# Optimization experiments

Measured on AMD Instinct MI355X. Metric: run time of the kernel, lower is better.

Reference implementation:

```python
import jax, jax.numpy as jnp
import numpy as np

N = 50000      # batch_num_nodes
E = 800000     # num edges (~avg degree 16)
A = 16         # num_atom_types
H = 64         # hidden dim
Z = 32         # latent dim
L_ENC = 2
L_DEC = 2
C_NORM = 16.0  # coordinate-update normalization (avg degree)


def _glorot(key, shape):
    fan = shape[-2] + shape[-1]
    return jax.random.normal(key, shape, dtype=jnp.float32) * np.float32(np.sqrt(2.0 / fan))


def _make_stack(key, n_layers, h_dim):
    # Stacked per-layer EGNN params: edge MLP (2 layers), coord head, node MLP (2 layers).
    def one(k):
        k0, k1, k2, k3, k4 = jax.random.split(k, 5)
        return (_glorot(k0, (2 * h_dim + 1, h_dim)), jnp.zeros((h_dim,), jnp.float32),
                _glorot(k1, (h_dim, h_dim)), jnp.zeros((h_dim,), jnp.float32),
                _glorot(k2, (h_dim, 1)),
                _glorot(k3, (2 * h_dim, h_dim)), jnp.zeros((h_dim,), jnp.float32),
                _glorot(k4, (h_dim, h_dim)), jnp.zeros((h_dim,), jnp.float32))
    parts = [one(k) for k in jax.random.split(key, n_layers)]
    return tuple(jnp.stack(p) for p in zip(*parts))


PARAM_NAMES = ["We1", "be1", "We2", "be2", "Wx", "Wn1", "bn1", "Wn2", "bn2"]


def setup_inputs() -> dict:
    key = jax.random.key(0)
    k = jax.random.split(key, 10)
    h = jax.random.normal(k[0], (N, A), dtype=jnp.float32)
    x = jax.random.normal(k[1], (N, 3), dtype=jnp.float32)
    edge_index = jax.random.randint(k[2], (2, E), 0, N, dtype=jnp.int32)
    inp = {"h": h, "x": x, "edge_index": edge_index,
           "W_emb": _glorot(k[3], (A, H)), "b_emb": jnp.zeros((H,), jnp.float32),
           "W_lat": _glorot(k[4], (H, Z)), "b_lat": jnp.zeros((Z,), jnp.float32),
           "W_up": _glorot(k[5], (Z, H)), "b_up": jnp.zeros((H,), jnp.float32),
           "W_out": _glorot(k[6], (H, A)), "b_out": jnp.zeros((A,), jnp.float32)}
    for n, p in zip(PARAM_NAMES, _make_stack(k[7], L_ENC, H)):
        inp["enc_" + n] = p
    for n, p in zip(PARAM_NAMES, _make_stack(k[8], L_DEC, H)):
        inp["dec_" + n] = p
    return inp


def _egnn_layer(h, x, src, dst, We1, be1, We2, be2, Wx, Wn1, bn1, Wn2, bn2):
    rel = x[src] - x[dst]                                    # [E, 3] gather
    d2 = jnp.sum(rel * rel, axis=-1, keepdims=True)          # [E, 1]
    ef = jnp.concatenate([h[src], h[dst], d2], axis=-1)      # [E, 2H+1]
    m = jax.nn.silu(jax.nn.silu(ef @ We1 + be1) @ We2 + be2)  # [E, H] per-edge message
    # equivariant coordinate update: scatter-add weighted relative vectors
    x = x + jax.ops.segment_sum(rel * (m @ Wx), dst, num_segments=N) / C_NORM
    agg = jnp.asarray(jax.ops.segment_sum(m, dst, num_segments=N))  # [N, H]
    h = h + jax.nn.silu(jnp.concatenate([h, agg], axis=-1) @ Wn1 + bn1) @ Wn2 + bn2
    return h, x


def reference(h, x, edge_index, W_emb, b_emb, W_lat, b_lat, W_up, b_up, W_out, b_out,
              enc_We1, enc_be1, enc_We2, enc_be2, enc_Wx, enc_Wn1, enc_bn1, enc_Wn2, enc_bn2,
              dec_We1, dec_be1, dec_We2, dec_be2, dec_Wx, dec_Wn1, dec_bn1, dec_Wn2, dec_bn2):
    src, dst = edge_index[0], edge_index[1]
    hh = h @ W_emb + b_emb
    for i in range(L_ENC):
        hh, x = _egnn_layer(hh, x, src, dst,
                            enc_We1[i], enc_be1[i], enc_We2[i], enc_be2[i], enc_Wx[i],
                            enc_Wn1[i], enc_bn1[i], enc_Wn2[i], enc_bn2[i])
    z = hh @ W_lat + b_lat                                   # latent [N, Z]
    hh = z @ W_up + b_up
    for i in range(L_DEC):
        hh, x = _egnn_layer(hh, x, src, dst,
                            dec_We1[i], dec_be1[i], dec_We2[i], dec_be2[i], dec_Wx[i],
                            dec_Wn1[i], dec_bn1[i], dec_Wn2[i], dec_bn2[i])
    h_rec = hh @ W_out + b_out                               # reconstructed atom-type logits
    return jnp.concatenate([h_rec, x], axis=-1)              # [N, A+3]
```

## Files before the change

### kernel.cpp

```cpp
#include <hip/hip_runtime.h>

#define NN 50000
#define NE 800000
#define MAXC 100000
#define EBLK 1024
#define SCB ((NN + 255) / 256)

__device__ __forceinline__ float silu_f(float v) {
    return v * __builtin_amdgcn_rcpf(1.f + __expf(-v));
}

typedef __bf16 bf16;
typedef bf16 v8bf __attribute__((ext_vector_type(8)));
typedef float v4f __attribute__((ext_vector_type(4)));

#define UNPACK8(dstv, ptr) { \
    float4 _a = reinterpret_cast<const float4*>(ptr)[0]; \
    float4 _b = reinterpret_cast<const float4*>(ptr)[1]; \
    dstv[0]=_a.x; dstv[1]=_a.y; dstv[2]=_a.z; dstv[3]=_a.w; \
    dstv[4]=_b.x; dstv[5]=_b.y; dstv[6]=_b.z; dstv[7]=_b.w; }

__global__ __launch_bounds__(256) void k_embed(
    const float* __restrict__ h_in, const float* __restrict__ x_in,
    const float* __restrict__ W, const float* __restrict__ b,
    float* __restrict__ h, float* __restrict__ xp)
{
    int t = blockIdx.x * 256 + threadIdx.x;
    if (t < NN * 4) { int n = t >> 2, c = t & 3; xp[t] = (c < 3) ? x_in[n * 3 + c] : 0.f; }
    int n = t >> 6, j = t & 63;
    const float* hr = h_in + n * 16;
    float acc = b[j];
#pragma unroll
    for (int k = 0; k < 16; k++) acc = fmaf(hr[k], W[k * 64 + j], acc);
    h[t] = acc;
}

__global__ __launch_bounds__(256) void k_prep_all(
    const float* __restrict__ eW1, const float* __restrict__ dW1,
    const float* __restrict__ eW2, const float* __restrict__ dW2,
    const float* __restrict__ eN1, const float* __restrict__ dN1,
    const float* __restrict__ eN2, const float* __restrict__ dN2,
    const float* __restrict__ Wlat, const float* __restrict__ Wup,
    bf16* __restrict__ We1h, bf16* __restrict__ We1l,
    bf16* __restrict__ We2h, bf16* __restrict__ We2l,
    bf16* __restrict__ Wn1h, bf16* __restrict__ Wn1l,
    bf16* __restrict__ Wn2h, bf16* __restrict__ Wn2l,
    bf16* __restrict__ Wlh,  bf16* __restrict__ Wll,
    bf16* __restrict__ Wuh,  bf16* __restrict__ Wul)
{
    int t = blockIdx.x * 256 + threadIdx.x;
    float w; int di; bf16 *Wh, *Wl;
    if (t < 98304) {
        const float *encW, *decW; int K, stride; int r;
        if (t < 32768)      { r = t;         encW = eW1; decW = dW1; K = 128; stride = 129 * 64; Wh = We1h; Wl = We1l; }
        else if (t < 49152) { r = t - 32768; encW = eW2; decW = dW2; K = 64;  stride = 64 * 64;  Wh = We2h; Wl = We2l; }
        else if (t < 81920) { r = t - 49152; encW = eN1; decW = dN1; K = 128; stride = 128 * 64; Wh = Wn1h; Wl = Wn1l; }
        else                { r = t - 81920; encW = eN2; decW = dN2; K = 64;  stride = 64 * 64;  Wh = Wn2h; Wl = Wn2l; }
        int per = K * 64;
        int li = r / per, rr = r - li * per;
        int k = rr >> 6, col = rr & 63;
        const float* Wsrc = (li < 2 ? encW : decW) + (li & 1) * stride;
        w = Wsrc[k * 64 + col];
        int kh = k >> 5, gg = (k >> 3) & 3, b = k & 7;
        di = li * per + (((kh * 4 + gg) * 64 + col) * 8 + b);
    } else if (t < 100352) {
        int r = t - 98304;
        int k = r >> 5, col = r & 31;
        w = Wlat[k * 32 + col];
        int kh = k >> 5, gg = (k >> 3) & 3, b = k & 7;
        di = ((kh * 4 + gg) * 32 + col) * 8 + b;
        Wh = Wlh; Wl = Wll;
    } else {
        int r = t - 100352;
        int k = r >> 6, col = r & 63;
        w = Wup[k * 64 + col];
        int gg = (k >> 3) & 3, b = k & 7;
        di = (gg * 64 + col) * 8 + b;
        Wh = Wuh; Wl = Wul;
    }
    bf16 hi = (bf16)w;
    Wh[di] = hi; Wl[di] = (bf16)(w - (float)hi);
}

__global__ __launch_bounds__(256) void k_zero_cnt(int* __restrict__ cnt)
{
    int t = blockIdx.x * 256 + threadIdx.x;
    if (t <= NN) cnt[t] = 0;
}

__global__ __launch_bounds__(256) void k_hist(const int* __restrict__ dst, int* __restrict__ cnt)
{
    int e = blockIdx.x * 256 + threadIdx.x;
    if (e < NE) atomicAdd(&cnt[dst[e]], 1);
}

__global__ __launch_bounds__(256) void k_blocksum(
    const int* __restrict__ cnt, int* __restrict__ bsum)
{
    int b = blockIdx.x, tid = threadIdx.x;
    int i = b * 256 + tid;
    int deg = (i < NN) ? cnt[i] : 0;
    int chk = (deg + 15) >> 4;
#pragma unroll
    for (int d = 1; d < 64; d <<= 1) { deg += __shfl_xor(deg, d); chk += __shfl_xor(chk, d); }
    __shared__ int sd[4], sc[4];
    int wv = tid >> 6;
    if ((tid & 63) == 0) { sd[wv] = deg; sc[wv] = chk; }
    __syncthreads();
    if (tid == 0) {
        bsum[b] = sd[0] + sd[1] + sd[2] + sd[3];
        bsum[SCB + b] = sc[0] + sc[1] + sc[2] + sc[3];
    }
}

__global__ __launch_bounds__(256) void k_scanbase(
    const int* __restrict__ bsum, int* __restrict__ bbase, int* __restrict__ ncptr)
{
    __shared__ int s[256], s2[256];
    int tid = threadIdx.x;
    int v  = (tid < SCB) ? bsum[tid] : 0;
    int v2 = (tid < SCB) ? bsum[SCB + tid] : 0;
    s[tid] = v; s2[tid] = v2;
    __syncthreads();
    for (int d = 1; d < 256; d <<= 1) {
        int u  = (tid >= d) ? s[tid - d] : 0;
        int u2 = (tid >= d) ? s2[tid - d] : 0;
        __syncthreads();
        s[tid] += u; s2[tid] += u2;
        __syncthreads();
    }
    if (tid < SCB) {
        bbase[tid]       = s[tid] - v;
        bbase[SCB + tid] = s2[tid] - v2;
    }
    if (tid == 255) *ncptr = s2[SCB - 1];
}

__global__ __launch_bounds__(256) void k_applyscan(
    int* __restrict__ cnt, const int* __restrict__ bbase,
    int* __restrict__ off, int* __restrict__ cur, int2* __restrict__ cpair)
{
    int b = blockIdx.x, tid = threadIdx.x;
    int i = b * 256 + tid;
    int deg = (i < NN) ? cnt[i] : 0;
    int chk = (deg + 15) >> 4;
    __shared__ int s[256], s2[256];
    s[tid] = deg; s2[tid] = chk;
    __syncthreads();
    for (int d = 1; d < 256; d <<= 1) {
        int u  = (tid >= d) ? s[tid - d] : 0;
        int u2 = (tid >= d) ? s2[tid - d] : 0;
        __syncthreads();
        s[tid] += u; s2[tid] += u2;
        __syncthreads();
    }
    if (i < NN) {
        int o = bbase[b] + s[tid] - deg;
        off[i] = o; cur[i] = o;
        int co = bbase[SCB + b] + s2[tid] - chk;
        int e = o + deg;
        int single = (deg <= 16) ? (1 << 25) : 0;
        for (int eb = o; eb < e; eb += 16) {
            int c = min(e - eb, 16);
            cpair[co++] = make_int2(i, eb | (c << 20) | single);
        }
    }
    if (i == 0) off[NN] = NE;
}

__global__ __launch_bounds__(256) void k_scatter(
    const int* __restrict__ dst, const int* __restrict__ srcArr,
    int* __restrict__ cur, int* __restrict__ srcp)
{
    int e = blockIdx.x * 256 + threadIdx.x;
    if (e < NE) { int p = atomicAdd(&cur[dst[e]], 1); srcp[p] = srcArr[e]; }
}

__global__ __launch_bounds__(256) void k_pq_mfma(
    const float* __restrict__ h,
    const bf16* __restrict__ We1h, const bf16* __restrict__ We1l,
    const float* __restrict__ be1,
    float* __restrict__ P, float* __restrict__ Q,
    float* __restrict__ agg, float* __restrict__ dxb)
{
    const int wv = threadIdx.x >> 6, lane = threadIdx.x & 63;
    const int g = lane >> 4, l15 = lane & 15;
    const int n0 = (blockIdx.x * 4 + wv) * 16;
    if (n0 >= NN) return;
    const int nrow = n0 + l15;

    v8bf Ah[2], Al[2];
#pragma unroll
    for (int kh = 0; kh < 2; kh++) {
        float v[8];
        UNPACK8(v, h + nrow * 64 + kh * 32 + g * 8);
#pragma unroll
        for (int b = 0; b < 8; b++) {
            bf16 hi = (bf16)v[b];
            Ah[kh][b] = hi; Al[kh][b] = (bf16)(v[b] - (float)hi);
        }
    }

    const v8bf* Bh = reinterpret_cast<const v8bf*>(We1h);
    const v8bf* Bl = reinterpret_cast<const v8bf*>(We1l);

    float be1v[4];
#pragma unroll
    for (int nt = 0; nt < 4; nt++) be1v[nt] = be1[l15 + 16 * nt];

#pragma unroll
    for (int nt = 0; nt < 4; nt++) {
        v4f ap = {0.f,0.f,0.f,0.f}, aq = {0.f,0.f,0.f,0.f};
#pragma unroll
        for (int kh = 0; kh < 2; kh++) {
            int fiP = (kh * 4 + g) * 64 + l15 + 16 * nt;
            int fiQ = ((kh + 2) * 4 + g) * 64 + l15 + 16 * nt;
            v8bf bph = Bh[fiP], bpl = Bl[fiP];
            v8bf bqh = Bh[fiQ], bql = Bl[fiQ];
            ap = __builtin_amdgcn_mfma_f32_16x16x32_bf16(Ah[kh], bph, ap, 0, 0, 0);
            ap = __builtin_amdgcn_mfma_f32_16x16x32_bf16(Ah[kh], bpl, ap, 0, 0, 0);
            ap = __builtin_amdgcn_mfma_f32_16x16x32_bf16(Al[kh], bph, ap, 0, 0, 0);
            aq = __builtin_amdgcn_mfma_f32_16x16x32_bf16(Ah[kh], bqh, aq, 0, 0, 0);
            aq = __builtin_amdgcn_mfma_f32_16x16x32_bf16(Ah[kh], bql, aq, 0, 0, 0);
            aq = __builtin_amdgcn_mfma_f32_16x16x32_bf16(Al[kh], bqh, aq, 0, 0, 0);
        }
#pragma unroll
        for (int i = 0; i < 4; i++) {
            int ro = (n0 + g * 4 + i) * 64 + l15 + 16 * nt;
            P[ro] = ap[i] + be1v[nt];
            Q[ro] = aq[i];
            agg[ro] = 0.f;
        }
    }
    {
        int nd = lane >> 2, cc = lane & 3;
        if (cc < 3) dxb[(n0 + nd) * 3 + cc] = 0.f;
    }
}

__device__ __forceinline__ void edge_compute(
    int n, int ct, int sg,
    const float4& xn, const float4& xs,
    const float4* pw, const float4* qv4,
    const v8bf* __restrict__ BHf, const v8bf* __restrict__ BLf,
    const float (&wdv)[2][8], const float (&be2v)[4], const float (&wxv)[4],
    int g, int l15, int lane,
    float* __restrict__ agg, float* __restrict__ dxb)
{
    float rx = xs.x - xn.x, ry = xs.y - xn.y, rz = xs.z - xn.z;
    float d2 = rx * rx + ry * ry + rz * rz;
    const float* pv = reinterpret_cast<const float*>(pw);
    const float* qv = reinterpret_cast<const float*>(qv4);

    v8bf Ah[2], Al[2];
#pragma unroll
    for (int kh = 0; kh < 2; kh++) {
#pragma unroll
        for (int b = 0; b < 8; b++) {
            float m1 = silu_f(pv[kh * 8 + b] + qv[kh * 8 + b] + d2 * wdv[kh][b]);
            bf16 hi = (bf16)m1;
            Ah[kh][b] = hi;
            Al[kh][b] = (bf16)(m1 - (float)hi);
        }
    }

    v4f acc[4];
#pragma unroll
    for (int nt = 0; nt < 4; nt++) {
        v4f a = {0.f, 0.f, 0.f, 0.f};
#pragma unroll
        for (int kh = 0; kh < 2; kh++) {
            int fi = (kh * 4 + g) * 64 + l15 + 16 * nt;
            v8bf bh = BHf[fi], bl = BLf[fi];
            a = __builtin_amdgcn_mfma_f32_16x16x32_bf16(Ah[kh], bh, a, 0, 0, 0);
            a = __builtin_amdgcn_mfma_f32_16x16x32_bf16(Ah[kh], bl, a, 0, 0, 0);
            a = __builtin_amdgcn_mfma_f32_16x16x32_bf16(Al[kh], bh, a, 0, 0, 0);
        }
        acc[nt] = a;
    }

    float aggv[4] = {0.f, 0.f, 0.f, 0.f};
    float dxx = 0.f, dxy = 0.f, dxz = 0.f;
#pragma unroll
    for (int i = 0; i < 4; i++) {
        bool valid = (g * 4 + i) < ct;
        float m0 = silu_f(acc[0][i] + be2v[0]); m0 = valid ? m0 : 0.f;
        float m1 = silu_f(acc[1][i] + be2v[1]); m1 = valid ? m1 : 0.f;
        float m2 = silu_f(acc[2][i] + be2v[2]); m2 = valid ? m2 : 0.f;
        float m3 = silu_f(acc[3][i] + be2v[3]); m3 = valid ? m3 : 0.f;
        aggv[0] += m0; aggv[1] += m1; aggv[2] += m2; aggv[3] += m3;
        float pd = m0 * wxv[0] + m1 * wxv[1] + m2 * wxv[2] + m3 * wxv[3];
        pd += __shfl_xor(pd, 1); pd += __shfl_xor(pd, 2);
        pd += __shfl_xor(pd, 4); pd += __shfl_xor(pd, 8);
        float rxe = __shfl(rx, g * 4 + i);
        float rye = __shfl(ry, g * 4 + i);
        float rze = __shfl(rz, g * 4 + i);
        if (l15 == 0) { dxx += rxe * pd; dxy += rye * pd; dxz += rze * pd; }
    }

#pragma unroll
    for (int nt = 0; nt < 4; nt++) {
        aggv[nt] += __shfl_xor(aggv[nt], 16);
        aggv[nt] += __shfl_xor(aggv[nt], 32);
    }
    if (lane < 16) {
        if (sg) {
#pragma unroll
            for (int nt = 0; nt < 4; nt++) agg[n * 64 + l15 + 16 * nt] = aggv[nt];
        } else {
#pragma unroll
            for (int nt = 0; nt < 4; nt++) unsafeAtomicAdd(&agg[n * 64 + l15 + 16 * nt], aggv[nt]);
        }
    }
    dxx += __shfl_xor(dxx, 16); dxx += __shfl_xor(dxx, 32);
    dxy += __shfl_xor(dxy, 16); dxy += __shfl_xor(dxy, 32);
    dxz += __shfl_xor(dxz, 16); dxz += __shfl_xor(dxz, 32);
    if (lane == 0) {
        if (sg) {
            dxb[n * 3 + 0] = dxx; dxb[n * 3 + 1] = dxy; dxb[n * 3 + 2] = dxz;
        } else {
            unsafeAtomicAdd(&dxb[n * 3 + 0], dxx);
            unsafeAtomicAdd(&dxb[n * 3 + 1], dxy);
            unsafeAtomicAdd(&dxb[n * 3 + 2], dxz);
        }
    }
}

__global__ __launch_bounds__(256) void k_edge_pipe(
    const int* __restrict__ srcp, const int2* __restrict__ cpair, const int* __restrict__ ncptr,
    const float* __restrict__ xp,
    const float* __restrict__ P, const float* __restrict__ Q,
    const float* __restrict__ Wd,
    const bf16* __restrict__ We2h, const bf16* __restrict__ We2l,
    const float* __restrict__ be2, const float* __restrict__ Wx,
    float* __restrict__ agg, float* __restrict__ dxb)
{
    const int wv = threadIdx.x >> 6, lane = threadIdx.x & 63;
    const int g = lane >> 4, l15 = lane & 15;
    const int Wstride = EBLK * 4;
    const int NC = *ncptr;
    int c0 = blockIdx.x * 4 + wv;
    if (c0 >= NC) return;

    const float4* xp4 = reinterpret_cast<const float4*>(xp);
    const float4* Pf4 = reinterpret_cast<const float4*>(P);
    const float4* Qf4 = reinterpret_cast<const float4*>(Q);
    const v8bf* BHf = reinterpret_cast<const v8bf*>(We2h);
    const v8bf* BLf = reinterpret_cast<const v8bf*>(We2l);

    float wdv[2][8];
    UNPACK8(wdv[0], Wd + g * 8);
    UNPACK8(wdv[1], Wd + 32 + g * 8);
    float be2v[4], wxv[4];
#pragma unroll
    for (int nt = 0; nt < 4; nt++) { be2v[nt] = be2[l15 + 16 * nt]; wxv[nt] = Wx[l15 + 16 * nt]; }

    int c1 = c0 + Wstride, c2 = c1 + Wstride, c3 = c2 + Wstride;
    int2 m0 = cpair[c0];
    int2 m1 = cpair[min(c1, NC - 1)];
    int2 m2 = cpair[min(c2, NC - 1)];
    int n0 = m0.x, eb0 = m0.y & 0xFFFFF, ct0 = (m0.y >> 20) & 31, sg0 = (m0.y >> 25) & 1;
    int n1 = m1.x, eb1 = m1.y & 0xFFFFF, ct1 = (m1.y >> 20) & 31, sg1 = (m1.y >> 25) & 1;
    int s0 = srcp[eb0 + min(l15, ct0 - 1)];
    int s1 = srcp[eb1 + min(l15, ct1 - 1)];
    float4 xn0 = xp4[n0], xn1 = xp4[n1];
    float4 xs0 = xp4[s0];
    float4 pw0[4], qv0[4];
    pw0[0] = Pf4[s0 * 16 + g * 2];     pw0[1] = Pf4[s0 * 16 + g * 2 + 1];
    pw0[2] = Pf4[s0 * 16 + 8 + g * 2]; pw0[3] = Pf4[s0 * 16 + 8 + g * 2 + 1];
    qv0[0] = Qf4[n0 * 16 + g * 2];     qv0[1] = Qf4[n0 * 16 + g * 2 + 1];
    qv0[2] = Qf4[n0 * 16 + 8 + g * 2]; qv0[3] = Qf4[n0 * 16 + 8 + g * 2 + 1];

    while (true) {
        float4 xs1 = xp4[s1];
        float4 pw1[4], qv1[4];
        pw1[0] = Pf4[s1 * 16 + g * 2];     pw1[1] = Pf4[s1 * 16 + g * 2 + 1];
        pw1[2] = Pf4[s1 * 16 + 8 + g * 2]; pw1[3] = Pf4[s1 * 16 + 8 + g * 2 + 1];
        qv1[0] = Qf4[n1 * 16 + g * 2];     qv1[1] = Qf4[n1 * 16 + g * 2 + 1];
        qv1[2] = Qf4[n1 * 16 + 8 + g * 2]; qv1[3] = Qf4[n1 * 16 + 8 + g * 2 + 1];
        int n2 = m2.x, eb2 = m2.y & 0xFFFFF, ct2 = (m2.y >> 20) & 31, sg2 = (m2.y >> 25) & 1;
        int s2 = srcp[eb2 + min(l15, ct2 - 1)];
        float4 xn2 = xp4[n2];
        int2 m3 = cpair[min(c3, NC - 1)];

        edge_compute(n0, ct0, sg0, xn0, xs0, pw0, qv0,
                     BHf, BLf, wdv, be2v, wxv, g, l15, lane, agg, dxb);

        c0 = c1; c1 = c2; c2 = c3; c3 += Wstride;
        n0 = n1; ct0 = ct1; sg0 = sg1; xn0 = xn1; xs0 = xs1;
#pragma unroll
        for (int j = 0; j < 4; j++) { pw0[j] = pw1[j]; qv0[j] = qv1[j]; }
        n1 = n2; ct1 = ct2; sg1 = sg2; s1 = s2; xn1 = xn2;
        m2 = m3;
        if (c0 >= NC) break;
    }
}

__global__ __launch_bounds__(256) void k_node_mfma(
    float* __restrict__ h, float* __restrict__ xp,
    float* __restrict__ agg, const float* __restrict__ dxb,
    const bf16* __restrict__ Wn1h, const bf16* __restrict__ Wn1l, const float* __restrict__ bn1,
    const bf16* __restrict__ Wn2h, const bf16* __restrict__ Wn2l, const float* __restrict__ bn2,
    int do_pq,
    const bf16* __restrict__ We1nh, const bf16* __restrict__ We1nl, const float* __restrict__ be1n,
    float* __restrict__ P, float* __restrict__ Q, float* __restrict__ dxbz,
    int do_lat,
    const bf16* __restrict__ Wlh, const bf16* __restrict__ Wll, const float* __restrict__ bl,
    const bf16* __restrict__ Wuh, const bf16* __restrict__ Wul, const float* __restrict__ bu)
{
    __shared__ float sh[4][16][68];
    __shared__ float su[4][16][68];

    const int wv = threadIdx.x >> 6, lane = threadIdx.x & 63;
    const int g = lane >> 4, l15 = lane & 15;
    const int n0 = (blockIdx.x * 4 + wv) * 16;
    if (n0 >= NN) return;

    const int nrow = n0 + l15;

    v8bf Ah[4], Al[4];
#pragma unroll
    for (int kh = 0; kh < 2; kh++) {
        float v[8];
        UNPACK8(v, h + nrow * 64 + kh * 32 + g * 8);
        *reinterpret_cast<float4*>(&sh[wv][l15][kh * 32 + g * 8])     = *reinterpret_cast<const float4*>(&v[0]);
        *reinterpret_cast<float4*>(&sh[wv][l15][kh * 32 + g * 8 + 4]) = *reinterpret_cast<const float4*>(&v[4]);
#pragma unroll
        for (int b = 0; b < 8; b++) {
            bf16 hi = (bf16)v[b];
            Ah[kh][b] = hi; Al[kh][b] = (bf16)(v[b] - (float)hi);
        }
    }
#pragma unroll
    for (int kh = 0; kh < 2; kh++) {
        float v[8];
        UNPACK8(v, agg + nrow * 64 + kh * 32 + g * 8);
#pragma unroll
        for (int b = 0; b < 8; b++) {
            bf16 hi = (bf16)v[b];
            Ah[2 + kh][b] = hi; Al[2 + kh][b] = (bf16)(v[b] - (float)hi);
        }
    }

    const v8bf* B1h = reinterpret_cast<const v8bf*>(Wn1h);
    const v8bf* B1l = reinterpret_cast<const v8bf*>(Wn1l);
    const v8bf* B2h = reinterpret_cast<const v8bf*>(Wn2h);
    const v8bf* B2l = reinterpret_cast<const v8bf*>(Wn2l);

    float bn1v[4];
#pragma unroll
    for (int nt = 0; nt < 4; nt++) bn1v[nt] = bn1[l15 + 16 * nt];
#pragma unroll
    for (int nt = 0; nt < 4; nt++) {
        v4f a = {0.f, 0.f, 0.f, 0.f};
#pragma unroll
        for (int kh = 0; kh < 4; kh++) {
            int fi = (kh * 4 + g) * 64 + l15 + 16 * nt;
            v8bf bh = B1h[fi], bl_ = B1l[fi];
            a = __builtin_amdgcn_mfma_f32_16x16x32_bf16(Ah[kh], bh, a, 0, 0, 0);
            a = __builtin_amdgcn_mfma_f32_16x16x32_bf16(Ah[kh], bl_, a, 0, 0, 0);
            a = __builtin_amdgcn_mfma_f32_16x16x32_bf16(Al[kh], bh, a, 0, 0, 0);
        }
#pragma unroll
        for (int i = 0; i < 4; i++)
            su[wv][g * 4 + i][l15 + 16 * nt] = silu_f(a[i] + bn1v[nt]);
    }
    asm volatile("s_waitcnt lgkmcnt(0)" ::: "memory");

    v8bf Uh[2], Ul[2];
#pragma unroll
    for (int kh = 0; kh < 2; kh++) {
        float v[8];
        *reinterpret_cast<float4*>(&v[0]) = *reinterpret_cast<const float4*>(&su[wv][l15][kh * 32 + g * 8]);
        *reinterpret_cast<float4*>(&v[4]) = *reinterpret_cast<const float4*>(&su[wv][l15][kh * 32 + g * 8 + 4]);
#pragma unroll
        for (int b = 0; b < 8; b++) {
            bf16 hi = (bf16)v[b];
            Uh[kh][b] = hi; Ul[kh][b] = (bf16)(v[b] - (float)hi);
        }
    }

    float bn2v[4];
#pragma unroll
    for (int nt = 0; nt < 4; nt++) bn2v[nt] = bn2[l15 + 16 * nt];
#pragma unroll
    for (int nt = 0; nt < 4; nt++) {
        v4f a = {0.f, 0.f, 0.f, 0.f};
#pragma unroll
        for (int kh = 0; kh < 2; kh++) {
            int fi = (kh * 4 + g) * 64 + l15 + 16 * nt;
            v8bf bh = B2h[fi], bl_ = B2l[fi];
            a = __builtin_amdgcn_mfma_f32_16x16x32_bf16(Uh[kh], bh, a, 0, 0, 0);
            a = __builtin_amdgcn_mfma_f32_16x16x32_bf16(Uh[kh], bl_, a, 0, 0, 0);
            a = __builtin_amdgcn_mfma_f32_16x16x32_bf16(Ul[kh], bh, a, 0, 0, 0);
        }
#pragma unroll
        for (int i = 0; i < 4; i++) {
            float hout = sh[wv][g * 4 + i][l15 + 16 * nt] + a[i] + bn2v[nt];
            if (!do_lat) h[(n0 + g * 4 + i) * 64 + l15 + 16 * nt] = hout;
            if (do_pq || do_lat) sh[wv][g * 4 + i][l15 + 16 * nt] = hout;
        }
    }

    {
        int nd = lane >> 2, cc = lane & 3;
        if (cc < 3) {
            xp[(n0 + nd) * 4 + cc] += dxb[(n0 + nd) * 3 + cc] * (1.f / 16.f);
            if (do_pq) dxbz[(n0 + nd) * 3 + cc] = 0.f;
        }
    }

    if (do_lat) {
        asm volatile("s_waitcnt lgkmcnt(0)" ::: "memory");
        v8bf Hh[2], Hl[2];
#pragma unroll
        for (int kh = 0; kh < 2; kh++) {
            float v[8];
            *reinterpret_cast<float4*>(&v[0]) = *reinterpret_cast<const float4*>(&sh[wv][l15][kh * 32 + g * 8]);
            *reinterpret_cast<float4*>(&v[4]) = *reinterpret_cast<const float4*>(&sh[wv][l15][kh * 32 + g * 8 + 4]);
#pragma unroll
            for (int b = 0; b < 8; b++) {
                bf16 hi = (bf16)v[b];
                Hh[kh][b] = hi; Hl[kh][b] = (bf16)(v[b] - (float)hi);
            }
        }
        const v8bf* BLh = reinterpret_cast<const v8bf*>(Wlh);
        const v8bf* BLl = reinterpret_cast<const v8bf*>(Wll);
#pragma unroll
        for (int nt = 0; nt < 2; nt++) {
            v4f a = {0.f, 0.f, 0.f, 0.f};
#pragma unroll
            for (int kh = 0; kh < 2; kh++) {
                int fi = (kh * 4 + g) * 32 + l15 + 16 * nt;
                v8bf bh = BLh[fi], bl_ = BLl[fi];
                a = __builtin_amdgcn_mfma_f32_16x16x32_bf16(Hh[kh], bh, a, 0, 0, 0);
                a = __builtin_amdgcn_mfma_f32_16x16x32_bf16(Hh[kh], bl_, a, 0, 0, 0);
                a = __builtin_amdgcn_mfma_f32_16x16x32_bf16(Hl[kh], bh, a, 0, 0, 0);
            }
            float blv = bl[l15 + 16 * nt];
#pragma unroll
            for (int i = 0; i < 4; i++)
                su[wv][g * 4 + i][l15 + 16 * nt] = a[i] + blv;
        }
        asm volatile("s_waitcnt lgkmcnt(0)" ::: "memory");

        v8bf Zh, Zl;
        {
            float v[8];
            *reinterpret_cast<float4*>(&v[0]) = *reinterpret_cast<const float4*>(&su[wv][l15][g * 8]);
            *reinterpret_cast<float4*>(&v[4]) = *reinterpret_cast<const float4*>(&su[wv][l15][g * 8 + 4]);
#pragma unroll
            for (int b = 0; b < 8; b++) {
                bf16 hi = (bf16)v[b];
                Zh[b] = hi; Zl[b] = (bf16)(v[b] - (float)hi);
            }
        }
        const v8bf* BUh = reinterpret_cast<const v8bf*>(Wuh);
        const v8bf* BUl = reinterpret_cast<const v8bf*>(Wul);
#pragma unroll
        for (int nt = 0; nt < 4; nt++) {
            v4f a = {0.f, 0.f, 0.f, 0.f};
            int fi = g * 64 + l15 + 16 * nt;
            v8bf bh = BUh[fi], bl_ = BUl[fi];
            a = __builtin_amdgcn_mfma_f32_16x16x32_bf16(Zh, bh, a, 0, 0, 0);
            a = __builtin_amdgcn_mfma_f32_16x16x32_bf16(Zh, bl_, a, 0, 0, 0);
            a = __builtin_amdgcn_mfma_f32_16x16x32_bf16(Zl, bh, a, 0, 0, 0);
            float buv = bu[l15 + 16 * nt];
#pragma unroll
            for (int i = 0; i < 4; i++) {
                float hout = a[i] + buv;
                h[(n0 + g * 4 + i) * 64 + l15 + 16 * nt] = hout;
                sh[wv][g * 4 + i][l15 + 16 * nt] = hout;
            }
        }
    }

    if (do_pq) {
        asm volatile("s_waitcnt lgkmcnt(0)" ::: "memory");
        v8bf Hh[2], Hl[2];
#pragma unroll
        for (int kh = 0; kh < 2; kh++) {
            float v[8];
            *reinterpret_cast<float4*>(&v[0]) = *reinterpret_cast<const float4*>(&sh[wv][l15][kh * 32 + g * 8]);
            *reinterpret_cast<float4*>(&v[4]) = *reinterpret_cast<const float4*>(&sh[wv][l15][kh * 32 + g * 8 + 4]);
#pragma unroll
            for (int b = 0; b < 8; b++) {
                bf16 hi = (bf16)v[b];
                Hh[kh][b] = hi; Hl[kh][b] = (bf16)(v[b] - (float)hi);
            }
        }
        const v8bf* Bh = reinterpret_cast<const v8bf*>(We1nh);
        const v8bf* Bl = reinterpret_cast<const v8bf*>(We1nl);
        float be1v[4];
#pragma unroll
        for (int nt = 0; nt < 4; nt++) be1v[nt] = be1n[l15 + 16 * nt];
#pragma unroll
        for (int nt = 0; nt < 4; nt++) {
            v4f ap = {0.f,0.f,0.f,0.f}, aq = {0.f,0.f,0.f,0.f};
#pragma unroll
            for (int kh = 0; kh < 2; kh++) {
                int fiP = (kh * 4 + g) * 64 + l15 + 16 * nt;
                int fiQ = ((kh + 2) * 4 + g) * 64 + l15 + 16 * nt;
                v8bf bph = Bh[fiP], bpl = Bl[fiP];
                v8bf bqh = Bh[fiQ], bql = Bl[fiQ];
                ap = __builtin_amdgcn_mfma_f32_16x16x32_bf16(Hh[kh], bph, ap, 0, 0, 0);
                ap = __builtin_amdgcn_mfma_f32_16x16x32_bf16(Hh[kh], bpl, ap, 0, 0, 0);
                ap = __builtin_amdgcn_mfma_f32_16x16x32_bf16(Hl[kh], bph, ap, 0, 0, 0);
                aq = __builtin_amdgcn_mfma_f32_16x16x32_bf16(Hh[kh], bqh, aq, 0, 0, 0);
                aq = __builtin_amdgcn_mfma_f32_16x16x32_bf16(Hh[kh], bql, aq, 0, 0, 0);
                aq = __builtin_amdgcn_mfma_f32_16x16x32_bf16(Hl[kh], bqh, aq, 0, 0, 0);
            }
#pragma unroll
            for (int i = 0; i < 4; i++) {
                int ro = (n0 + g * 4 + i) * 64 + l15 + 16 * nt;
                P[ro] = ap[i] + be1v[nt];
                Q[ro] = aq[i];
                agg[ro] = 0.f;
            }
        }
    }
}

__global__ __launch_bounds__(256) void k_out(
    const float* __restrict__ h, const float* __restrict__ xp,
    const float* __restrict__ Wo, const float* __restrict__ bo,
    float* __restrict__ out)
{
    int t = blockIdx.x * 256 + threadIdx.x;
    if (t >= NN * 19) return;
    int n = t / 19, c = t - n * 19;
    if (c < 16) {
        const float4* hr = reinterpret_cast<const float4*>(h + n * 64);
        float acc = bo[c];
#pragma unroll
        for (int kb = 0; kb < 16; kb++) {
            float4 hv = hr[kb];
            acc = fmaf(hv.x, Wo[(4 * kb + 0) * 16 + c], acc);
            acc = fmaf(hv.y, Wo[(4 * kb + 1) * 16 + c], acc);
            acc = fmaf(hv.z, Wo[(4 * kb + 2) * 16 + c], acc);
            acc = fmaf(hv.w, Wo[(4 * kb + 3) * 16 + c], acc);
        }
        out[t] = acc;
    } else {
        out[t] = xp[n * 4 + (c - 16)];
    }
}

extern "C" void kernel_launch(void* const* d_in, const int* in_sizes, int n_in,
                              void* d_out, int out_size, void* d_ws, size_t ws_size,
                              hipStream_t stream)
{
    const float* h_in  = (const float*)d_in[0];
    const float* x_in  = (const float*)d_in[1];
    const int*   ei    = (const int*)d_in[2];
    const float* W_emb = (const float*)d_in[3];
    const float* b_emb = (const float*)d_in[4];
    const float* W_lat = (const float*)d_in[5];
    const float* b_lat = (const float*)d_in[6];
    const float* W_up  = (const float*)d_in[7];
    const float* b_up  = (const float*)d_in[8];
    const float* W_out = (const float*)d_in[9];
    const float* b_out = (const float*)d_in[10];
    const float* encp[9]; const float* decp[9];
    for (int i = 0; i < 9; i++) { encp[i] = (const float*)d_in[11 + i]; decp[i] = (const float*)d_in[20 + i]; }

    const int* src = ei;
    const int* dst = ei + NE;

    float* ws  = (float*)d_ws;
    float* h   = ws;
    float* xp  = h + NN * 64;
    float* P   = xp + NN * 4;
    float* Q   = P + NN * 64;
    float* agg = Q + NN * 64;
    float* dxb = agg + NN * 64;
    int* off   = (int*)(dxb + NN * 3);
    int* cur   = off + (NN + 1);
    int* bsum  = cur + (NN + 1);
    int* bbase = bsum + 2 * SCB;
    int* srcp  = bbase + 2 * SCB;
    int* ncptr = srcp + NE;
    int2* cpair = (int2*)(ncptr + 2);
    bf16* We1h = (bf16*)(cpair + MAXC);
    bf16* We1l = We1h + 4 * 8192;
    bf16* We2h = We1l + 4 * 8192;
    bf16* We2l = We2h + 4 * 4096;
    bf16* Wn1h = We2l + 4 * 4096;
    bf16* Wn1l = Wn1h + 4 * 8192;
    bf16* Wn2h = Wn1l + 4 * 8192;
    bf16* Wn2l = Wn2h + 4 * 4096;
    bf16* Wlh  = Wn2l + 4 * 4096;
    bf16* Wll  = Wlh + 2048;
    bf16* Wuh  = Wll + 2048;
    bf16* Wul  = Wuh + 2048;

    k_zero_cnt<<<(NN + 256) / 256, 256, 0, stream>>>(cur);
    k_hist<<<NE / 256, 256, 0, stream>>>(dst, cur);
    k_blocksum<<<SCB, 256, 0, stream>>>(cur, bsum);
    k_scanbase<<<1, 256, 0, stream>>>(bsum, bbase, ncptr);
    k_applyscan<<<SCB, 256, 0, stream>>>(cur, bbase, off, cur, cpair);
    k_scatter<<<NE / 256, 256, 0, stream>>>(dst, src, cur, srcp);
    k_prep_all<<<400, 256, 0, stream>>>(encp[0], decp[0], encp[2], decp[2],
                                        encp[5], decp[5], encp[7], decp[7],
                                        W_lat, W_up,
                                        We1h, We1l, We2h, We2l, Wn1h, Wn1l, Wn2h, Wn2l,
                                        Wlh, Wll, Wuh, Wul);

    k_embed<<<(NN * 64) / 256, 256, 0, stream>>>(h_in, x_in, W_emb, b_emb, h, xp);

    const int NODE_GRID = (NN / 16 + 3) / 4;

    k_pq_mfma<<<NODE_GRID, 256, 0, stream>>>(h, We1h, We1l, encp[1], P, Q, agg, dxb);

    for (int L = 0; L < 4; ++L) {
        const float** pp = (L < 2) ? encp : decp;
        int li = (L < 2) ? L : L - 2;
        const float* We1 = pp[0] + li * 129 * 64;
        const float* be2 = pp[3] + li * 64;
        const float* Wx  = pp[4] + li * 64;
        const float* bn1 = pp[6] + li * 64;
        const float* bn2 = pp[8] + li * 64;

        k_edge_pipe<<<EBLK, 256, 0, stream>>>(srcp, cpair, ncptr,
                                              xp, P, Q, We1 + 128 * 64,
                                              We2h + L * 4096, We2l + L * 4096,
                                              be2, Wx, agg, dxb);

        int do_pq = (L < 3) ? 1 : 0;
        int do_lat = (L == 1) ? 1 : 0;
        int Ln = L + 1;
        const float* be1n = bn1;
        if (do_pq) be1n = (Ln < 2 ? encp[1] : decp[1]) + ((Ln < 2 ? Ln : Ln - 2)) * 64;

        k_node_mfma<<<NODE_GRID, 256, 0, stream>>>(h, xp, agg, dxb,
                                                   Wn1h + L * 8192, Wn1l + L * 8192, bn1,
                                                   Wn2h + L * 4096, Wn2l + L * 4096, bn2,
                                                   do_pq,
                                                   We1h + Ln * 8192, We1l + Ln * 8192, be1n,
                                                   P, Q, dxb,
                                                   do_lat, Wlh, Wll, b_lat, Wuh, Wul, b_up);
    }

    k_out<<<(NN * 19 + 255) / 256, 256, 0, stream>>>(h, xp, W_out, b_out, (float*)d_out);
}
```

Baseline: 585.9 us.

## Fuse embedding into first PQ kernel and output projection into last node kernel

```diff
diff --git a/kernel.cpp b/kernel.cpp
--- a/kernel.cpp
+++ b/kernel.cpp
@@ -19,21 +19,6 @@
     float4 _b = reinterpret_cast<const float4*>(ptr)[1]; \
     dstv[0]=_a.x; dstv[1]=_a.y; dstv[2]=_a.z; dstv[3]=_a.w; \
     dstv[4]=_b.x; dstv[5]=_b.y; dstv[6]=_b.z; dstv[7]=_b.w; }
-
-__global__ __launch_bounds__(256) void k_embed(
-    const float* __restrict__ h_in, const float* __restrict__ x_in,
-    const float* __restrict__ W, const float* __restrict__ b,
-    float* __restrict__ h, float* __restrict__ xp)
-{
-    int t = blockIdx.x * 256 + threadIdx.x;
-    if (t < NN * 4) { int n = t >> 2, c = t & 3; xp[t] = (c < 3) ? x_in[n * 3 + c] : 0.f; }
-    int n = t >> 6, j = t & 63;
-    const float* hr = h_in + n * 16;
-    float acc = b[j];
-#pragma unroll
-    for (int k = 0; k < 16; k++) acc = fmaf(hr[k], W[k * 64 + j], acc);
-    h[t] = acc;
-}
 
 __global__ __launch_bounds__(256) void k_prep_all(
     const float* __restrict__ eW1, const float* __restrict__ dW1,
@@ -41,12 +26,15 @@
     const float* __restrict__ eN1, const float* __restrict__ dN1,
     const float* __restrict__ eN2, const float* __restrict__ dN2,
     const float* __restrict__ Wlat, const float* __restrict__ Wup,
+    const float* __restrict__ Wemb, const float* __restrict__ Wout,
     bf16* __restrict__ We1h, bf16* __restrict__ We1l,
     bf16* __restrict__ We2h, bf16* __restrict__ We2l,
     bf16* __restrict__ Wn1h, bf16* __restrict__ Wn1l,
     bf16* __restrict__ Wn2h, bf16* __restrict__ Wn2l,
     bf16* __restrict__ Wlh,  bf16* __restrict__ Wll,
-    bf16* __restrict__ Wuh,  bf16* __restrict__ Wul)
+    bf16* __restrict__ Wuh,  bf16* __restrict__ Wul,
+    bf16* __restrict__ Wembh, bf16* __restrict__ Wembl,
+    bf16* __restrict__ Wouth, bf16* __restrict__ Woutl)
 {
     int t = blockIdx.x * 256 + threadIdx.x;
     float w; int di; bf16 *Wh, *Wl;
@@ -70,22 +58,31 @@
         int kh = k >> 5, gg = (k >> 3) & 3, b = k & 7;
         di = ((kh * 4 + gg) * 32 + col) * 8 + b;
         Wh = Wlh; Wl = Wll;
-    } else {
+    } else if (t < 102400) {
         int r = t - 100352;
         int k = r >> 6, col = r & 63;
         w = Wup[k * 64 + col];
         int gg = (k >> 3) & 3, b = k & 7;
         di = (gg * 64 + col) * 8 + b;
         Wh = Wuh; Wl = Wul;
-    }
+    } else if (t < 104448) {
+        int r = t - 102400;
+        int gg = r >> 9, col = (r >> 3) & 63, b = r & 7;
+        int k = gg * 8 + b;
+        w = (k < 16) ? Wemb[k * 64 + col] : 0.f;
+        di = r;
+        Wh = Wembh; Wl = Wembl;
+    } else if (t < 105472) {
+        int r = t - 104448;
+        int kh4g = r >> 7, col = (r >> 3) & 15, b = r & 7;
+        int kh = kh4g >> 2, gg = kh4g & 3;
+        int k = kh * 32 + gg * 8 + b;
+        w = Wout[k * 16 + col];
+        di = r;
+        Wh = Wouth; Wl = Woutl;
+    } else return;
     bf16 hi = (bf16)w;
     Wh[di] = hi; Wl[di] = (bf16)(w - (float)hi);
-}
-
-__global__ __launch_bounds__(256) void k_zero_cnt(int* __restrict__ cnt)
-{
-    int t = blockIdx.x * 256 + threadIdx.x;
-    if (t <= NN) cnt[t] = 0;
 }
 
 __global__ __launch_bounds__(256) void k_hist(const int* __restrict__ dst, int* __restrict__ cnt)
@@ -177,23 +174,67 @@
 }
 
 __global__ __launch_bounds__(256) void k_pq_mfma(
-    const float* __restrict__ h,
+    const float* __restrict__ h_in, const float* __restrict__ x_in,
+    const bf16* __restrict__ Wembh, const bf16* __restrict__ Wembl, const float* __restrict__ bemb,
+    float* __restrict__ h, float* __restrict__ xp,
     const bf16* __restrict__ We1h, const bf16* __restrict__ We1l,
     const float* __restrict__ be1,
     float* __restrict__ P, float* __restrict__ Q,
     float* __restrict__ agg, float* __restrict__ dxb)
 {
+    __shared__ float sh[4][16][68];
     const int wv = threadIdx.x >> 6, lane = threadIdx.x & 63;
     const int g = lane >> 4, l15 = lane & 15;
     const int n0 = (blockIdx.x * 4 + wv) * 16;
     if (n0 >= NN) return;
     const int nrow = n0 + l15;
 
+    v8bf Eh, El;
+    if (g < 2) {
+        float ev[8];
+        UNPACK8(ev, h_in + nrow * 16 + g * 8);
+#pragma unroll
+        for (int b = 0; b < 8; b++) {
+            bf16 hi = (bf16)ev[b];
+            Eh[b] = hi; El[b] = (bf16)(ev[b] - (float)hi);
+        }
+    } else {
+#pragma unroll
+        for (int b = 0; b < 8; b++) { Eh[b] = (bf16)0.f; El[b] = (bf16)0.f; }
+    }
+    {
+        const v8bf* BEh = reinterpret_cast<const v8bf*>(Wembh);
+        const v8bf* BEl = reinterpret_cast<const v8bf*>(Wembl);
+#pragma unroll
+        for (int nt = 0; nt < 4; nt++) {
+            v4f a = {0.f, 0.f, 0.f, 0.f};
+            int fi = g * 64 + l15 + 16 * nt;
+            v8bf bh = BEh[fi], bl_ = BEl[fi];
+            a = __builtin_amdgcn_mfma_f32_16x16x32_bf16(Eh, bh, a, 0, 0, 0);
+            a = __builtin_amdgcn_mfma_f32_16x16x32_bf16(Eh, bl_, a, 0, 0, 0);
+            a = __builtin_amdgcn_mfma_f32_16x16x32_bf16(El, bh, a, 0, 0, 0);
+            float bev = bemb[l15 + 16 * nt];
+#pragma unroll
+            for (int i = 0; i < 4; i++) {
+                float hv = a[i] + bev;
+                h[(n0 + g * 4 + i) * 64 + l15 + 16 * nt] = hv;
+                sh[wv][g * 4 + i][l15 + 16 * nt] = hv;
+            }
+        }
+    }
+    {
+        int nd = lane >> 2, cc = lane & 3;
+        xp[(n0 + nd) * 4 + cc] = (cc < 3) ? x_in[(n0 + nd) * 3 + cc] : 0.f;
+        if (cc < 3) dxb[(n0 + nd) * 3 + cc] = 0.f;
+    }
+    asm volatile("s_waitcnt lgkmcnt(0)" ::: "memory");
+
     v8bf Ah[2], Al[2];
 #pragma unroll
     for (int kh = 0; kh < 2; kh++) {
         float v[8];
-        UNPACK8(v, h + nrow * 64 + kh * 32 + g * 8);
+        *reinterpret_cast<float4*>(&v[0]) = *reinterpret_cast<const float4*>(&sh[wv][l15][kh * 32 + g * 8]);
+        *reinterpret_cast<float4*>(&v[4]) = *reinterpret_cast<const float4*>(&sh[wv][l15][kh * 32 + g * 8 + 4]);
 #pragma unroll
         for (int b = 0; b < 8; b++) {
             bf16 hi = (bf16)v[b];
@@ -231,10 +272,6 @@
             Q[ro] = aq[i];
             agg[ro] = 0.f;
         }
-    }
-    {
-        int nd = lane >> 2, cc = lane & 3;
-        if (cc < 3) dxb[(n0 + nd) * 3 + cc] = 0.f;
     }
 }
 
@@ -406,7 +443,10 @@
     float* __restrict__ P, float* __restrict__ Q, float* __restrict__ dxbz,
     int do_lat,
     const bf16* __restrict__ Wlh, const bf16* __restrict__ Wll, const float* __restrict__ bl,
-    const bf16* __restrict__ Wuh, const bf16* __restrict__ Wul, const float* __restrict__ bu)
+    const bf16* __restrict__ Wuh, const bf16* __restrict__ Wul, const float* __restrict__ bu,
+    int do_out,
+    const bf16* __restrict__ Woh, const bf16* __restrict__ Wol, const float* __restrict__ bo,
+    float* __restrict__ out)
 {
     __shared__ float sh[4][16][68];
     __shared__ float su[4][16][68];
@@ -497,16 +537,21 @@
 #pragma unroll
         for (int i = 0; i < 4; i++) {
             float hout = sh[wv][g * 4 + i][l15 + 16 * nt] + a[i] + bn2v[nt];
-            if (!do_lat) h[(n0 + g * 4 + i) * 64 + l15 + 16 * nt] = hout;
-            if (do_pq || do_lat) sh[wv][g * 4 + i][l15 + 16 * nt] = hout;
+            if (!do_lat && !do_out) h[(n0 + g * 4 + i) * 64 + l15 + 16 * nt] = hout;
+            if (do_pq || do_lat || do_out) sh[wv][g * 4 + i][l15 + 16 * nt] = hout;
         }
     }
 
     {
         int nd = lane >> 2, cc = lane & 3;
         if (cc < 3) {
-            xp[(n0 + nd) * 4 + cc] += dxb[(n0 + nd) * 3 + cc] * (1.f / 16.f);
-            if (do_pq) dxbz[(n0 + nd) * 3 + cc] = 0.f;
+            float xnew = xp[(n0 + nd) * 4 + cc] + dxb[(n0 + nd) * 3 + cc] * (1.f / 16.f);
+            if (do_out) {
+                out[(n0 + nd) * 19 + 16 + cc] = xnew;
+            } else {
+                xp[(n0 + nd) * 4 + cc] = xnew;
+                if (do_pq) dxbz[(n0 + nd) * 3 + cc] = 0.f;
+            }
         }
     }
 
@@ -619,30 +664,36 @@
             }
         }
     }
-}
-
-__global__ __launch_bounds__(256) void k_out(
-    const float* __restrict__ h, const float* __restrict__ xp,
-    const float* __restrict__ Wo, const float* __restrict__ bo,
-    float* __restrict__ out)
-{
-    int t = blockIdx.x * 256 + threadIdx.x;
-    if (t >= NN * 19) return;
-    int n = t / 19, c = t - n * 19;
-    if (c < 16) {
-        const float4* hr = reinterpret_cast<const float4*>(h + n * 64);
-        float acc = bo[c];
-#pragma unroll
-        for (int kb = 0; kb < 16; kb++) {
-            float4 hv = hr[kb];
-            acc = fmaf(hv.x, Wo[(4 * kb + 0) * 16 + c], acc);
-            acc = fmaf(hv.y, Wo[(4 * kb + 1) * 16 + c], acc);
-            acc = fmaf(hv.z, Wo[(4 * kb + 2) * 16 + c], acc);
-            acc = fmaf(hv.w, Wo[(4 * kb + 3) * 16 + c], acc);
-        }
-        out[t] = acc;
-    } else {
-        out[t] = xp[n * 4 + (c - 16)];
+
+    if (do_out) {
+        asm volatile("s_waitcnt lgkmcnt(0)" ::: "memory");
+        v8bf Hh[2], Hl[2];
+#pragma unroll
+        for (int kh = 0; kh < 2; kh++) {
+            float v[8];
+            *reinterpret_cast<float4*>(&v[0]) = *reinterpret_cast<const float4*>(&sh[wv][l15][kh * 32 + g * 8]);
+            *reinterpret_cast<float4*>(&v[4]) = *reinterpret_cast<const float4*>(&sh[wv][l15][kh * 32 + g * 8 + 4]);
+#pragma unroll
+            for (int b = 0; b < 8; b++) {
+                bf16 hi = (bf16)v[b];
+                Hh[kh][b] = hi; Hl[kh][b] = (bf16)(v[b] - (float)hi);
+            }
+        }
+        const v8bf* BOh = reinterpret_cast<const v8bf*>(Woh);
+        const v8bf* BOl = reinterpret_cast<const v8bf*>(Wol);
+        float bov = bo[l15];
+        v4f a = {0.f, 0.f, 0.f, 0.f};
+#pragma unroll
+        for (int kh = 0; kh < 2; kh++) {
+            int fi = (kh * 4 + g) * 16 + l15;
+            v8bf bh = BOh[fi], bl_ = BOl[fi];
+            a = __builtin_amdgcn_mfma_f32_16x16x32_bf16(Hh[kh], bh, a, 0, 0, 0);
+            a = __builtin_amdgcn_mfma_f32_16x16x32_bf16(Hh[kh], bl_, a, 0, 0, 0);
+            a = __builtin_amdgcn_mfma_f32_16x16x32_bf16(Hl[kh], bh, a, 0, 0, 0);
+        }
+#pragma unroll
+        for (int i = 0; i < 4; i++)
+            out[(n0 + g * 4 + i) * 19 + l15] = a[i] + bov;
     }
 }
 
@@ -693,24 +744,27 @@
     bf16* Wll  = Wlh + 2048;
     bf16* Wuh  = Wll + 2048;
     bf16* Wul  = Wuh + 2048;
-
-    k_zero_cnt<<<(NN + 256) / 256, 256, 0, stream>>>(cur);
+    bf16* Wembh = Wul + 2048;
+    bf16* Wembl = Wembh + 2048;
+    bf16* Wouth = Wembl + 2048;
+    bf16* Woutl = Wouth + 1024;
+
+    hipMemsetAsync(cur, 0, (NN + 1) * sizeof(int), stream);
     k_hist<<<NE / 256, 256, 0, stream>>>(dst, cur);
     k_blocksum<<<SCB, 256, 0, stream>>>(cur, bsum);
     k_scanbase<<<1, 256, 0, stream>>>(bsum, bbase, ncptr);
     k_applyscan<<<SCB, 256, 0, stream>>>(cur, bbase, off, cur, cpair);
     k_scatter<<<NE / 256, 256, 0, stream>>>(dst, src, cur, srcp);
-    k_prep_all<<<400, 256, 0, stream>>>(encp[0], decp[0], encp[2], decp[2],
+    k_prep_all<<<412, 256, 0, stream>>>(encp[0], decp[0], encp[2], decp[2],
                                         encp[5], decp[5], encp[7], decp[7],
-                                        W_lat, W_up,
+                                        W_lat, W_up, W_emb, W_out,
                                         We1h, We1l, We2h, We2l, Wn1h, Wn1l, Wn2h, Wn2l,
-                                        Wlh, Wll, Wuh, Wul);
-
-    k_embed<<<(NN * 64) / 256, 256, 0, stream>>>(h_in, x_in, W_emb, b_emb, h, xp);
+                                        Wlh, Wll, Wuh, Wul, Wembh, Wembl, Wouth, Woutl);
 
     const int NODE_GRID = (NN / 16 + 3) / 4;
 
-    k_pq_mfma<<<NODE_GRID, 256, 0, stream>>>(h, We1h, We1l, encp[1], P, Q, agg, dxb);
+    k_pq_mfma<<<NODE_GRID, 256, 0, stream>>>(h_in, x_in, Wembh, Wembl, b_emb, h, xp,
+                                             We1h, We1l, encp[1], P, Q, agg, dxb);
 
     for (int L = 0; L < 4; ++L) {
         const float** pp = (L < 2) ? encp : decp;
@@ -728,6 +782,7 @@
 
         int do_pq = (L < 3) ? 1 : 0;
         int do_lat = (L == 1) ? 1 : 0;
+        int do_out = (L == 3) ? 1 : 0;
         int Ln = L + 1;
         const float* be1n = bn1;
         if (do_pq) be1n = (Ln < 2 ? encp[1] : decp[1]) + ((Ln < 2 ? Ln : Ln - 2)) * 64;
@@ -736,10 +791,10 @@
                                                    Wn1h + L * 8192, Wn1l + L * 8192, bn1,
                                                    Wn2h + L * 4096, Wn2l + L * 4096, bn2,
                                                    do_pq,
-                                                   We1h + Ln * 8192, We1l + Ln * 8192, be1n,
+                                                   We1h + (do_pq ? Ln : 0) * 8192,
+                                                   We1l + (do_pq ? Ln : 0) * 8192, be1n,
                                                    P, Q, dxb,
-                                                   do_lat, Wlh, Wll, b_lat, Wuh, Wul, b_up);
-    }
-
-    k_out<<<(NN * 19 + 255) / 256, 256, 0, stream>>>(h, xp, W_out, b_out, (float*)d_out);
-}
+                                                   do_lat, Wlh, Wll, b_lat, Wuh, Wul, b_up,
+                                                   do_out, Wouth, Woutl, b_out, (float*)d_out);
+    }
+}
```

Result: faster. 557.6 us (median of 2 runs) (-4.8%).
